# Kernel tuning notes

Measured on AMD Instinct MI355X. Metric: run time of the kernel, lower is better.

Reference implementation:

```python
import jax, jax.numpy as jnp
import numpy as np

NEG_SLOPE = 0.2


def gat_conv(x, src, dst, W, asrc, adst, b):
    """Single-head PyG-style GATConv with self-loops.
    x: [N, din], src/dst: [E] int, W: [din, d], asrc/adst: [d], b: [d]."""
    N = x.shape[0]
    h = x @ W  # [N, d]
    alpha_s = h @ asrc  # [N]
    alpha_d = h @ adst  # [N]
    # add self loops so every node has at least one incoming edge
    loop = jnp.arange(N, dtype=src.dtype)
    srcf = jnp.concatenate([src, loop])
    dstf = jnp.concatenate([dst, loop])
    e = jax.nn.leaky_relu(alpha_s[srcf] + alpha_d[dstf], NEG_SLOPE)  # [E+N]
    m = jax.ops.segment_max(e, dstf, num_segments=N)
    ex = jnp.exp(e - m[dstf])
    denom = jax.ops.segment_sum(ex, dstf, num_segments=N)
    alpha = ex / denom[dstf]
    out = jax.ops.segment_sum(h[srcf] * alpha[:, None], dstf, num_segments=N)
    return out + b


def sdgnn_forward(x, edges, Wg, a_src, a_dst, bg, W1, b1, W2, b2):
    L = Wg.shape[0]
    R = Wg.shape[1]
    for l in range(L):
        feats = [x]
        for r in range(R):
            feats.append(gat_conv(x, edges[r, 0], edges[r, 1],
                                  Wg[l, r], a_src[l, r], a_dst[l, r], bg[l, r]))
        combined = jnp.concatenate(feats, axis=1)  # [N, 5*d]
        x = jnp.tanh(combined @ W1[l] + b1[l]) @ W2[l] + b2[l]
    return x


def setup_inputs() -> dict:
    key = jax.random.key(0)
    ks = jax.random.split(key, 8)
    N, D, E, L, R = 100000, 64, 1000000, 2, 4
    scale = 0.15  # ~kaiming for d=64
    x = jax.random.normal(ks[0], (N, D), dtype=jnp.float32)
    edges = jax.random.randint(ks[1], (R, 2, E), 0, N, dtype=jnp.int64)
    Wg = jax.random.normal(ks[2], (L, R, D, D), dtype=jnp.float32) * scale
    a_src = jax.random.normal(ks[3], (L, R, D), dtype=jnp.float32) * scale
    a_dst = jax.random.normal(ks[4], (L, R, D), dtype=jnp.float32) * scale
    bg = jnp.zeros((L, R, D), dtype=jnp.float32)
    W1 = jax.random.normal(ks[5], (L, 5 * D, D), dtype=jnp.float32) * 0.08
    b1 = jnp.zeros((L, D), dtype=jnp.float32)
    W2 = jax.random.normal(ks[6], (L, D, D), dtype=jnp.float32) * scale
    b2 = jnp.zeros((L, D), dtype=jnp.float32)
    return {"x": x, "edges": edges, "Wg": Wg, "a_src": a_src, "a_dst": a_dst,
            "bg": bg, "W1": W1, "b1": b1, "W2": W2, "b2": b2}


def reference(x, edges, Wg, a_src, a_dst, bg, W1, b1, W2, b2):
    return sdgnn_forward(x, edges, Wg, a_src, a_dst, bg, W1, b1, W2, b2)
```

## Files before the change

### kernel.cpp

```cpp
#include <hip/hip_runtime.h>
#include <hip/hip_bf16.h>
#include <math.h>

#define DD 64
#define RREL 4
#define LLAY 2
#define NEG_SLOPE 0.2f
#define EPB 4096
#define BSH 10
#define BSZ 1024

typedef __attribute__((ext_vector_type(8))) short short8;
typedef __attribute__((ext_vector_type(4))) short short4v;
typedef __attribute__((ext_vector_type(4))) float float4v;

__device__ __forceinline__ float lrelu(float x) { return x > 0.f ? x : NEG_SLOPE * x; }

__device__ __forceinline__ unsigned short f2bf(float f) {
    unsigned int u = __float_as_uint(f);
    return (unsigned short)((u + 0x7FFFu + ((u >> 16) & 1u)) >> 16);
}
__device__ __forceinline__ float bf2f(unsigned short u) {
    return __uint_as_float((unsigned int)u << 16);
}

__global__ void k_wvec(const float* __restrict__ Wg, const float* __restrict__ asrc,
                       const float* __restrict__ adst, float* __restrict__ wsrc,
                       float* __restrict__ wdst) {
    int idx = blockIdx.x * blockDim.x + threadIdx.x;
    if (idx >= LLAY * RREL * DD) return;
    int k = idx & 63;
    int lr = idx >> 6;
    const float* W = Wg + (size_t)lr * DD * DD;
    const float* as = asrc + lr * DD;
    const float* ad = adst + lr * DD;
    float s1 = 0.f, s2 = 0.f;
#pragma unroll
    for (int j = 0; j < DD; j++) {
        float w = W[k * DD + j];
        s1 += w * as[j];
        s2 += w * ad[j];
    }
    wsrc[idx] = s1;
    wdst[idx] = s2;
}

__global__ void k_prep(const float* __restrict__ Wg, const float* __restrict__ W1,
                       const float* __restrict__ W2, unsigned short* __restrict__ WgT,
                       unsigned short* __restrict__ W1T, unsigned short* __restrict__ W2T) {
    int idx = blockIdx.x * blockDim.x + threadIdx.x;
    if (idx < 8 * 4096) {
        int lr = idx >> 12, rem = idx & 4095, n = rem >> 6, k = rem & 63;
        WgT[idx] = f2bf(Wg[(size_t)lr * 4096 + k * 64 + n]);
    } else if (idx < 32768 + 2 * 64 * 320) {
        int i = idx - 32768;
        int l = i / 20480, rem = i % 20480, n = rem / 320, kk = rem % 320;
        int src;
        if (kk < 64) src = kk;
        else {
            int r = (kk - 64) >> 6, f = (kk - 64) & 63;
            src = 64 + r * 64 + ((f & 3) * 16) + (f >> 2);
        }
        W1T[i] = f2bf(W1[(size_t)l * 20480 + src * 64 + n]);
    } else if (idx < 32768 + 40960 + 2 * 4096) {
        int i = idx - 73728;
        int l = i >> 12, rem = i & 4095, n = rem >> 6, k = rem & 63;
        W2T[i] = f2bf(W2[(size_t)l * 4096 + k * 64 + n]);
    }
}

__global__ void k_copy_x(const float* __restrict__ x, unsigned short* __restrict__ combined,
                         int N) {
    int i = blockIdx.x * blockDim.x + threadIdx.x;
    if (i >= N * 32) return;
    int row = i >> 5, c2 = i & 31;
    float2 v = *(const float2*)(x + (size_t)row * DD + c2 * 2);
    unsigned int p = (unsigned int)f2bf(v.x) | ((unsigned int)f2bf(v.y) << 16);
    *(unsigned int*)(combined + (size_t)row * 320 + c2 * 2) = p;
}

__global__ void k_zero(int* __restrict__ p, int n) {
    int i = blockIdx.x * blockDim.x + threadIdx.x;
    if (i < n) p[i] = 0;
}

__global__ __launch_bounds__(256) void k_bhist(const int* __restrict__ edges,
                                               int* __restrict__ btot, int E, int NB) {
    int r = blockIdx.y;
    int e0 = blockIdx.x * EPB;
    int t = threadIdx.x;
    __shared__ int lh[128];
    for (int i = t; i < 128; i += 256) lh[i] = 0;
    __syncthreads();
    const int* dstp = edges + (size_t)r * 2 * E + E;
#pragma unroll
    for (int i = 0; i < EPB / 256; i++) {
        int e = e0 + t + 256 * i;
        if (e < E) atomicAdd(&lh[dstp[e] >> BSH], 1);
    }
    __syncthreads();
    for (int i = t; i < NB; i += 256) {
        int c = lh[i];
        if (c) atomicAdd(&btot[r * NB + i], c);
    }
}

__global__ void k_bscan(const int* __restrict__ btot, int* __restrict__ bucketoff,
                        int* __restrict__ bpos, int* __restrict__ csr_ptr, int N, int E, int NB) {
    int r = threadIdx.x;
    if (r >= RREL) return;
    int run = 0;
    for (int b = 0; b < NB; b++) {
        bucketoff[r * (NB + 1) + b] = run;
        bpos[r * NB + b] = run;
        run += btot[r * NB + b];
    }
    bucketoff[r * (NB + 1) + NB] = run;
    csr_ptr[(size_t)r * (N + 1) + N] = E;
}

__global__ __launch_bounds__(256) void k_binscatter(const int* __restrict__ edges,
                                                    int* __restrict__ bpos,
                                                    unsigned int* __restrict__ packed, int E,
                                                    int NB) {
    int r = blockIdx.y;
    int e0 = blockIdx.x * EPB;
    int t = threadIdx.x;
    __shared__ int lh[128], lbase[128];
    for (int i = t; i < 128; i += 256) lh[i] = 0;
    __syncthreads();
    const int* srcp = edges + (size_t)r * 2 * E;
    const int* dstp = srcp + E;
    int md[EPB / 256], ms[EPB / 256];
#pragma unroll
    for (int i = 0; i < EPB / 256; i++) {
        int e = e0 + t + 256 * i;
        int d = -1, s = 0;
        if (e < E) {
            d = dstp[e];
            s = srcp[e];
            atomicAdd(&lh[d >> BSH], 1);
        }
        md[i] = d;
        ms[i] = s;
    }
    __syncthreads();
    for (int i = t; i < NB; i += 256) {
        int c = lh[i];
        lbase[i] = c ? atomicAdd(&bpos[r * NB + i], c) : 0;
        lh[i] = 0;
    }
    __syncthreads();
#pragma unroll
    for (int i = 0; i < EPB / 256; i++) {
        if (md[i] >= 0) {
            int b = md[i] >> BSH;
            int p = lbase[b] + atomicAdd(&lh[b], 1);
            packed[(size_t)r * E + p] =
                ((unsigned int)(md[i] & (BSZ - 1)) << 17) | (unsigned int)ms[i];
        }
    }
}

__global__ __launch_bounds__(256) void k_bucket_sort(const unsigned int* __restrict__ packed,
                                                     const int* __restrict__ bucketoff,
                                                     int* __restrict__ csr_ptr,
                                                     int* __restrict__ csr_src, int N, int E,
                                                     int NB) {
    int r = blockIdx.y, b = blockIdx.x;
    int t = threadIdx.x;
    __shared__ int pos[BSZ];
    __shared__ int tsum[256];
    int base = bucketoff[r * (NB + 1) + b];
    int cnt = bucketoff[r * (NB + 1) + b + 1] - base;
    const unsigned int* pk = packed + (size_t)r * E + base;
    for (int i = t; i < BSZ; i += 256) pos[i] = 0;
    __syncthreads();
    for (int i = t; i < cnt; i += 256) atomicAdd(&pos[pk[i] >> 17], 1);
    __syncthreads();
    int v[4];
    int s = 0;
#pragma unroll
    for (int i = 0; i < 4; i++) {
        v[i] = pos[t * 4 + i];
        s += v[i];
    }
    tsum[t] = s;
    __syncthreads();
    for (int off = 1; off < 256; off <<= 1) {
        int add = (t >= off) ? tsum[t - off] : 0;
        __syncthreads();
        tsum[t] += add;
        __syncthreads();
    }
    int run = tsum[t] - s;
    __syncthreads();
#pragma unroll
    for (int i = 0; i < 4; i++) {
        int node_l = t * 4 + i;
        pos[node_l] = run;
        int node = b * BSZ + node_l;
        if (node < N) csr_ptr[(size_t)r * (N + 1) + node] = base + run;
        run += v[i];
    }
    __syncthreads();
    for (int i = t; i < cnt; i += 256) {
        unsigned int p = pk[i];
        int d = p >> 17;
        int sidx = p & 0x1FFFF;
        int loc = atomicAdd(&pos[d], 1);
        csr_src[(size_t)r * E + base + loc] = sidx;
    }
}


__global__ __launch_bounds__(256, 3) void k_hgemm(const unsigned short* __restrict__ X,
                                                  const unsigned short* __restrict__ WgTl,
                                                  const float* __restrict__ wsrcl,
                                                  const float* __restrict__ wdstl,
                                                  unsigned short* __restrict__ h4,
                                                  float* __restrict__ as4,
                                                  float* __restrict__ ad4, int N) {
    __shared__ __align__(16) unsigned short Xb[256][72];
    __shared__ __align__(16) unsigned short Wb[64][72];
    __shared__ float wsS[4][64], wdS[4][64];
    int tid = threadIdx.x, wave = tid >> 6, lane = tid & 63;
    int l15 = lane & 15, q = lane >> 4;
    int row0 = blockIdx.x * 256;
#pragma unroll
    for (int i = 0; i < 8; i++) {
        int f = tid + 256 * i;
        int rr = f >> 3, seg = f & 7;
        int grow = row0 + rr;
        short8 v = (short8){0, 0, 0, 0, 0, 0, 0, 0};
        if (grow < N) v = *(const short8*)(X + (size_t)grow * 320 + seg * 8);
        *(short8*)&Xb[rr][seg * 8] = v;
    }
    wsS[tid >> 6][tid & 63] = wsrcl[tid];
    wdS[tid >> 6][tid & 63] = wdstl[tid];
    __syncthreads();
    short8 afr[4][2];
#pragma unroll
    for (int mt = 0; mt < 4; mt++)
#pragma unroll
        for (int ks = 0; ks < 2; ks++)
            afr[mt][ks] = *(const short8*)&Xb[wave * 64 + mt * 16 + l15][ks * 32 + q * 8];
    {
        int grow = row0 + tid;
        float s[4] = {0.f, 0.f, 0.f, 0.f}, d[4] = {0.f, 0.f, 0.f, 0.f};
#pragma unroll
        for (int seg = 0; seg < 8; seg++) {
            short8 v = *(const short8*)&Xb[tid][seg * 8];
#pragma unroll
            for (int j = 0; j < 8; j++) {
                float xv = bf2f((unsigned short)v[j]);
                int k = seg * 8 + j;
#pragma unroll
                for (int r = 0; r < 4; r++) {
                    s[r] += xv * wsS[r][k];
                    d[r] += xv * wdS[r][k];
                }
            }
        }
        if (grow < N) {
#pragma unroll
            for (int r = 0; r < 4; r++) {
                as4[(size_t)r * N + grow] = s[r];
                ad4[(size_t)r * N + grow] = d[r];
            }
        }
    }
    for (int r = 0; r < 4; r++) {
        __syncthreads();
#pragma unroll
        for (int i = 0; i < 2; i++) {
            int f = tid + 256 * i;
            int n = f >> 3, seg = f & 7;
            *(short8*)&Wb[n][seg * 8] = *(const short8*)(WgTl + r * 4096 + n * 64 + seg * 8);
        }
        __syncthreads();
        short8 bfr[4][2];
#pragma unroll
        for (int nt = 0; nt < 4; nt++)
#pragma unroll
            for (int ks = 0; ks < 2; ks++)
                bfr[nt][ks] = *(const short8*)&Wb[nt * 16 + l15][ks * 32 + q * 8];
        float4v acc[4][4];
#pragma unroll
        for (int mt = 0; mt < 4; mt++)
#pragma unroll
            for (int nt = 0; nt < 4; nt++) acc[mt][nt] = (float4v){0.f, 0.f, 0.f, 0.f};
#pragma unroll
        for (int mt = 0; mt < 4; mt++)
#pragma unroll
            for (int nt = 0; nt < 4; nt++) {
                acc[mt][nt] = __builtin_amdgcn_mfma_f32_16x16x32_bf16(afr[mt][0], bfr[nt][0],
                                                                     acc[mt][nt], 0, 0, 0);
                acc[mt][nt] = __builtin_amdgcn_mfma_f32_16x16x32_bf16(afr[mt][1], bfr[nt][1],
                                                                     acc[mt][nt], 0, 0, 0);
            }
        unsigned short* hr = h4 + (size_t)r * N * 64;
#pragma unroll
        for (int mt = 0; mt < 4; mt++) {
            int rowb = row0 + wave * 64 + mt * 16 + q * 4;
#pragma unroll
            for (int reg = 0; reg < 4; reg++) {
                int row = rowb + reg;
                if (row < N) {
                    short4v sv;
                    sv[0] = (short)f2bf(acc[mt][0][reg]);
                    sv[1] = (short)f2bf(acc[mt][1][reg]);
                    sv[2] = (short)f2bf(acc[mt][2][reg]);
                    sv[3] = (short)f2bf(acc[mt][3][reg]);
                    *(short4v*)&hr[(size_t)row * 64 + l15 * 4] = sv;
                }
            }
        }
    }
}

template <bool BFOUT>
__global__ __launch_bounds__(256, 3) void k_mlp(const unsigned short* __restrict__ X,
                                                const unsigned short* __restrict__ W1Tl,
                                                const float* __restrict__ b1,
                                                const unsigned short* __restrict__ W2Tl,
                                                const float* __restrict__ b2,
                                                unsigned short* __restrict__ Ybf,
                                                float* __restrict__ Yf, int ldy, int N) {
    __shared__ __align__(16) unsigned short Xb[256][72];
    __shared__ __align__(16) unsigned short Wb[64][72];
    int tid = threadIdx.x, wave = tid >> 6, lane = tid & 63;
    int l15 = lane & 15, q = lane >> 4;
    int row0 = blockIdx.x * 256;
    float4v acc[4][4];
#pragma unroll
    for (int mt = 0; mt < 4; mt++)
#pragma unroll
        for (int nt = 0; nt < 4; nt++) acc[mt][nt] = (float4v){0.f, 0.f, 0.f, 0.f};
    for (int kc = 0; kc < 320; kc += 64) {
        __syncthreads();
#pragma unroll
        for (int i = 0; i < 8; i++) {
            int f = tid + 256 * i;
            int rr = f >> 3, seg = f & 7;
            int grow = row0 + rr;
            short8 v = (short8){0, 0, 0, 0, 0, 0, 0, 0};
            if (grow < N) v = *(const short8*)(X + (size_t)grow * 320 + kc + seg * 8);
            *(short8*)&Xb[rr][seg * 8] = v;
        }
#pragma unroll
        for (int i = 0; i < 2; i++) {
            int f = tid + 256 * i;
            int n = f >> 3, seg = f & 7;
            *(short8*)&Wb[n][seg * 8] = *(const short8*)(W1Tl + n * 320 + kc + seg * 8);
        }
        __syncthreads();
        short8 bfr[4][2];
#pragma unroll
        for (int nt = 0; nt < 4; nt++)
#pragma unroll
            for (int ks = 0; ks < 2; ks++)
                bfr[nt][ks] = *(const short8*)&Wb[nt * 16 + l15][ks * 32 + q * 8];
#pragma unroll
        for (int mt = 0; mt < 4; mt++) {
            short8 a0 = *(const short8*)&Xb[wave * 64 + mt * 16 + l15][q * 8];
            short8 a1 = *(const short8*)&Xb[wave * 64 + mt * 16 + l15][32 + q * 8];
#pragma unroll
            for (int nt = 0; nt < 4; nt++) {
                acc[mt][nt] =
                    __builtin_amdgcn_mfma_f32_16x16x32_bf16(a0, bfr[nt][0], acc[mt][nt], 0, 0, 0);
                acc[mt][nt] =
                    __builtin_amdgcn_mfma_f32_16x16x32_bf16(a1, bfr[nt][1], acc[mt][nt], 0, 0, 0);
            }
        }
    }
    __syncthreads();
#pragma unroll
    for (int mt = 0; mt < 4; mt++) {
        int rlb = wave * 64 + mt * 16 + q * 4;
#pragma unroll
        for (int reg = 0; reg < 4; reg++) {
#pragma unroll
            for (int nt = 0; nt < 4; nt++) {
                int n = nt * 16 + l15;
                Xb[rlb + reg][n] = f2bf(tanhf(acc[mt][nt][reg] + b1[n]));
            }
        }
    }
#pragma unroll
    for (int i = 0; i < 2; i++) {
        int f = tid + 256 * i;
        int n = f >> 3, seg = f & 7;
        *(short8*)&Wb[n][seg * 8] = *(const short8*)(W2Tl + n * 64 + seg * 8);
    }
    __syncthreads();
    short8 bfr[4][2];
#pragma unroll
    for (int nt = 0; nt < 4; nt++)
#pragma unroll
        for (int ks = 0; ks < 2; ks++)
            bfr[nt][ks] = *(const short8*)&Wb[nt * 16 + l15][ks * 32 + q * 8];
    float4v acc2[4][4];
#pragma unroll
    for (int mt = 0; mt < 4; mt++)
#pragma unroll
        for (int nt = 0; nt < 4; nt++) acc2[mt][nt] = (float4v){0.f, 0.f, 0.f, 0.f};
#pragma unroll
    for (int mt = 0; mt < 4; mt++) {
        short8 a0 = *(const short8*)&Xb[wave * 64 + mt * 16 + l15][q * 8];
        short8 a1 = *(const short8*)&Xb[wave * 64 + mt * 16 + l15][32 + q * 8];
#pragma unroll
        for (int nt = 0; nt < 4; nt++) {
            acc2[mt][nt] =
                __builtin_amdgcn_mfma_f32_16x16x32_bf16(a0, bfr[nt][0], acc2[mt][nt], 0, 0, 0);
            acc2[mt][nt] =
                __builtin_amdgcn_mfma_f32_16x16x32_bf16(a1, bfr[nt][1], acc2[mt][nt], 0, 0, 0);
        }
    }
#pragma unroll
    for (int mt = 0; mt < 4; mt++) {
        int rowb = row0 + wave * 64 + mt * 16 + q * 4;
#pragma unroll
        for (int reg = 0; reg < 4; reg++) {
            int row = rowb + reg;
            if (row < N) {
#pragma unroll
                for (int nt = 0; nt < 4; nt++) {
                    int n = nt * 16 + l15;
                    float v = acc2[mt][nt][reg] + b2[n];
                    if (BFOUT)
                        Ybf[(size_t)row * ldy + n] = f2bf(v);
                    else
                        Yf[(size_t)row * ldy + n] = v;
                }
            }
        }
    }
}

__device__ void gat_node_fullwave(int node, const int* __restrict__ csr_ptr,
                                  const int* __restrict__ csr_src,
                                  const unsigned short* __restrict__ h,
                                  const float* __restrict__ as_,
                                  const float* __restrict__ ad_, float bgv,
                                  unsigned short* __restrict__ out, int ldo, int lane) {
    float adv = ad_[node];
    float e_self = lrelu(as_[node] + adv);
    int beg = csr_ptr[node], end = csr_ptr[node + 1];
    int cnt = end - beg;

    if (cnt <= 64) {
        int s = 0;
        float e_lane = -3.0e38f;
        if (lane < cnt) {
            s = csr_src[beg + lane];
            e_lane = lrelu(as_[s] + adv);
        }
        float m = fmaxf(e_lane, e_self);
#pragma unroll
        for (int off = 32; off; off >>= 1) m = fmaxf(m, __shfl_xor(m, off));
        float p = (lane < cnt) ? expf(e_lane - m) : 0.f;
        float ssum = p;
#pragma unroll
        for (int off = 32; off; off >>= 1) ssum += __shfl_xor(ssum, off);
        float p_self = expf(e_self - m);
        float inv = 1.f / (ssum + p_self);
        float alpha = p * inv;
        float acc = p_self * inv * bf2f(h[(size_t)node * DD + lane]);
        for (int j0 = 0; j0 < cnt; ++j0) {
            int ss = __shfl(s, j0);
            float aa = __shfl(alpha, j0);
            acc += aa * bf2f(h[(size_t)ss * DD + lane]);
        }
        out[(size_t)node * ldo + lane] = f2bf(acc + bgv);
        return;
    }

    float m = e_self;
    for (int j = beg + lane; j < end; j += 64) m = fmaxf(m, lrelu(as_[csr_src[j]] + adv));
#pragma unroll
    for (int off = 32; off; off >>= 1) m = fmaxf(m, __shfl_xor(m, off));
    float ssum = 0.f;
    for (int j = beg + lane; j < end; j += 64) ssum += expf(lrelu(as_[csr_src[j]] + adv) - m);
#pragma unroll
    for (int off = 32; off; off >>= 1) ssum += __shfl_xor(ssum, off);
    ssum += expf(e_self - m);
    float inv = 1.f / ssum;
    float acc = expf(e_self - m) * inv * bf2f(h[(size_t)node * DD + lane]);
    for (int j0 = beg; j0 < end; j0 += 64) {
        int j = j0 + lane;
        int s = 0;
        float alpha = 0.f;
        if (j < end) {
            s = csr_src[j];
            alpha = expf(lrelu(as_[s] + adv) - m) * inv;
        }
        int c = end - j0;
        if (c > 64) c = 64;
        for (int t = 0; t < c; ++t) {
            int ss = __shfl(s, t);
            float aa = __shfl(alpha, t);
            acc += aa * bf2f(h[(size_t)ss * DD + lane]);
        }
    }
    out[(size_t)node * ldo + lane] = f2bf(acc + bgv);
}

__global__ __launch_bounds__(256) void k_gat(const int* __restrict__ csr_ptr4,
                                             const int* __restrict__ csr_src4,
                                             const unsigned short* __restrict__ h4,
                                             const float* __restrict__ as4,
                                             const float* __restrict__ ad4,
                                             const float* __restrict__ bg4,
                                             unsigned short* __restrict__ outbase, int ldo,
                                             int N, int E) {
    __shared__ int lsa_s[4][2][32];
    __shared__ float lsa_p[4][2][32];
    int lb = blockIdx.x;
    int r = (lb & 7) >> 1;
    int idx = ((lb >> 3) << 1) + (lb & 1);
    int wave = threadIdx.x >> 6, lane = threadIdx.x & 63;
    int half = lane >> 5, lh = lane & 31;
    int nodeA = idx * 8 + wave * 2;
    if (nodeA >= N) return;
    int node = nodeA + half;
    bool act = node < N;

    const int* csr_ptr = csr_ptr4 + (size_t)r * (N + 1);
    const int* csr_src = csr_src4 + (size_t)r * E;
    const unsigned short* h = h4 + (size_t)r * N * 64;
    const float* as_ = as4 + (size_t)r * N;
    const float* ad_ = ad4 + (size_t)r * N;
    const float* bg = bg4 + (size_t)r * DD;
    unsigned short* out = outbase + (size_t)64 * r;

    int beg = 0, cnt = 0;
    if (act) {
        beg = csr_ptr[node];
        cnt = csr_ptr[node + 1] - beg;
    }
    int vmax = __builtin_amdgcn_readfirstlane(max(cnt, __shfl_xor(cnt, 32)));

    if (vmax <= 32) {
        bool in = lh < cnt;
        int s = 0;
        if (in) s = csr_src[beg + lh];
        lsa_s[wave][half][lh] = s;
        float adv = act ? ad_[node] : 0.f;
        float asl = in ? as_[s] : 0.f;
        float e_self = act ? lrelu(as_[node] + adv) : 0.f;
        float p = in ? __expf(lrelu(asl + adv)) : 0.f;
        lsa_p[wave][half][lh] = p;
        float p_self = __expf(e_self);

        const char* hb = (const char*)h;
        unsigned lane4 = (unsigned)(lh << 2);
        unsigned int hvs = 0;
        if (act) hvs = *(const unsigned int*)(hb + (((unsigned)node) << 7) + lane4);

        float ax0 = 0.f, ay0 = 0.f, ax1 = 0.f, ay1 = 0.f;
        const int* sp = &lsa_s[wave][half][0];
        const float* pp = &lsa_p[wave][half][0];
        for (int j0 = 0; j0 < vmax; j0 += 8) {
#pragma unroll
            for (int g = 0; g < 2; g++) {
                if (j0 + g * 4 < vmax) {
#pragma unroll
                    for (int u = 0; u < 4; u++) {
                        int sv = sp[j0 + g * 4 + u];
                        unsigned voff = ((unsigned)sv << 7) + lane4;
                        unsigned int hv = *(const unsigned int*)(hb + voff);
                        float pw = pp[j0 + g * 4 + u];
                        if (u & 1) {
                            ax1 += pw * __uint_as_float(hv << 16);
                            ay1 += pw * __uint_as_float(hv & 0xffff0000u);
                        } else {
                            ax0 += pw * __uint_as_float(hv << 16);
                            ay0 += pw * __uint_as_float(hv & 0xffff0000u);
                        }
                    }
                }
            }
        }
        float ssum = p;
#pragma unroll
        for (int off = 16; off; off >>= 1) ssum += __shfl_xor(ssum, off);
        float inv = __builtin_amdgcn_rcpf(ssum + p_self);

        if (act) {
            int f0 = 2 * lh;
            float bx = bg[((f0 & 3) << 4) | (f0 >> 2)];
            float by = bg[(((f0 + 1) & 3) << 4) | (f0 >> 2)];
            float ox = (ax0 + ax1 + p_self * __uint_as_float(hvs << 16)) * inv + bx;
            float oy = (ay0 + ay1 + p_self * __uint_as_float(hvs & 0xffff0000u)) * inv + by;
            unsigned int pck = (unsigned int)f2bf(ox) | ((unsigned int)f2bf(oy) << 16);
            *(unsigned int*)(out + (size_t)node * ldo + f0) = pck;
        }
        return;
    }

    float bgv = bg[((lane & 3) << 4) | (lane >> 2)];
    if (nodeA < N)
        gat_node_fullwave(nodeA, csr_ptr, csr_src, h, as_, ad_, bgv, out, ldo, lane);
    if (nodeA + 1 < N)
        gat_node_fullwave(nodeA + 1, csr_ptr, csr_src, h, as_, ad_, bgv, out, ldo, lane);
}

extern "C" void kernel_launch(void* const* d_in, const int* in_sizes, int n_in,
                              void* d_out, int out_size, void* d_ws, size_t ws_size,
                              hipStream_t stream) {
    const float* x = (const float*)d_in[0];
    const int* edges = (const int*)d_in[1];
    const float* Wg = (const float*)d_in[2];
    const float* a_src = (const float*)d_in[3];
    const float* a_dst = (const float*)d_in[4];
    const float* bg = (const float*)d_in[5];
    const float* W1 = (const float*)d_in[6];
    const float* b1 = (const float*)d_in[7];
    const float* W2 = (const float*)d_in[8];
    const float* b2 = (const float*)d_in[9];
    float* out = (float*)d_out;

    const int N = in_sizes[0] / DD;
    const int E = in_sizes[1] / (2 * RREL);
    const int NB = (N + BSZ - 1) >> BSH;

    size_t off = 0;
    auto alloc = [&](size_t bytes) {
        size_t o = off;
        off = (off + bytes + 255) & ~(size_t)255;
        return o;
    };
    char* ws = (char*)d_ws;
    unsigned short* combined = (unsigned short*)(ws + alloc((size_t)N * 320 * 2));
    unsigned short* h4 = (unsigned short*)(ws + alloc((size_t)4 * N * 64 * 2));
    float* wsrc = (float*)(ws + alloc(LLAY * RREL * DD * 4));
    float* wdst = (float*)(ws + alloc(LLAY * RREL * DD * 4));
    unsigned short* WgT = (unsigned short*)(ws + alloc(8 * 4096 * 2));
    unsigned short* W1T = (unsigned short*)(ws + alloc(2 * 64 * 320 * 2));
    unsigned short* W2T = (unsigned short*)(ws + alloc(2 * 4096 * 2));
    int* btot = (int*)(ws + alloc((size_t)RREL * NB * 4));
    int* bucketoff = (int*)(ws + alloc((size_t)RREL * (NB + 1) * 4));
    int* bpos = (int*)(ws + alloc((size_t)RREL * NB * 4));
    unsigned int* packed = (unsigned int*)(ws + alloc((size_t)RREL * E * 4));
    int* csr_ptr = (int*)(ws + alloc((size_t)RREL * (N + 1) * 4));
    int* csr_src = (int*)(ws + alloc((size_t)RREL * E * 4));
    (void)ws_size;
    float* as4 = (float*)packed;
    float* ad4 = as4 + (size_t)4 * N;

    const int ebblocks = (E + EPB - 1) / EPB;

    k_zero<<<dim3((RREL * NB + 255) / 256), dim3(256), 0, stream>>>(btot, RREL * NB);
    k_wvec<<<dim3(2), dim3(256), 0, stream>>>(Wg, a_src, a_dst, wsrc, wdst);
    k_prep<<<dim3(320), dim3(256), 0, stream>>>(Wg, W1, W2, WgT, W1T, W2T);
    k_copy_x<<<dim3((N * 32 + 255) / 256), dim3(256), 0, stream>>>(x, combined, N);
    k_bhist<<<dim3(ebblocks, RREL), dim3(256), 0, stream>>>(edges, btot, E, NB);
    k_bscan<<<dim3(1), dim3(64), 0, stream>>>(btot, bucketoff, bpos, csr_ptr, N, E, NB);
    k_binscatter<<<dim3(ebblocks, RREL), dim3(256), 0, stream>>>(edges, bpos, packed, E, NB);
    k_bucket_sort<<<dim3(NB, RREL), dim3(256), 0, stream>>>(packed, bucketoff, csr_ptr, csr_src,
                                                            N, E, NB);

    const int gemm_blocks = (N + 255) / 256;
    const int bpr = (N + 7) / 8;
    const int gat_grid = 8 * ((bpr + 1) / 2);

    for (int l = 0; l < LLAY; l++) {
        k_hgemm<<<dim3(gemm_blocks), dim3(256), 0, stream>>>(
            combined, WgT + (size_t)l * 4 * 4096, wsrc + l * 256, wdst + l * 256, h4, as4, ad4, N);
        k_gat<<<dim3(gat_grid), dim3(256), 0, stream>>>(
            csr_ptr, csr_src, h4, as4, ad4, bg + (size_t)l * RREL * DD,
            combined + 64, 320, N, E);
        if (l == LLAY - 1) {
            k_mlp<false><<<dim3(gemm_blocks), dim3(256), 0, stream>>>(
                combined, W1T + (size_t)l * 20480, b1 + l * DD, W2T + (size_t)l * 4096,
                b2 + l * DD, nullptr, out, DD, N);
        } else {
            k_mlp<true><<<dim3(gemm_blocks), dim3(256), 0, stream>>>(
                combined, W1T + (size_t)l * 20480, b1 + l * DD, W2T + (size_t)l * 4096,
                b2 + l * DD, combined, nullptr, 320, N);
        }
    }
}
```

Before: 504.3 us.

## Map 16 nodes per wave with 4 lanes per node in GAT aggregation

Restructures the GAT aggregation kernel so each wave handles 16 destination nodes, with 4 lanes per node each loading 32 bytes (two 16-byte vectors) of the bf16 feature row and keeping 16 accumulators. Previously each half-wave handled one node with 4-byte loads per lane. The aim is wider gather loads, fewer waves and better latency hiding per gathered edge. The cost is higher register pressure, more serial edge iterations per lane, and a wave-wide max degree that makes waves with skewed degrees do more work or fall back to the full-wave path for all 16 nodes. Output stores are now non-temporal 16-byte writes.

```diff
diff --git a/kernel.cpp b/kernel.cpp
--- a/kernel.cpp
+++ b/kernel.cpp
@@ -13,6 +13,7 @@
 typedef __attribute__((ext_vector_type(8))) short short8;
 typedef __attribute__((ext_vector_type(4))) short short4v;
 typedef __attribute__((ext_vector_type(4))) float float4v;
+typedef __attribute__((ext_vector_type(4))) unsigned int uint4v;
 
 __device__ __forceinline__ float lrelu(float x) { return x > 0.f ? x : NEG_SLOPE * x; }
 
@@ -22,6 +23,10 @@
 }
 __device__ __forceinline__ float bf2f(unsigned short u) {
     return __uint_as_float((unsigned int)u << 16);
+}
+__device__ __forceinline__ float bflo(unsigned int u) { return __uint_as_float(u << 16); }
+__device__ __forceinline__ float bfhi(unsigned int u) {
+    return __uint_as_float(u & 0xffff0000u);
 }
 
 __global__ void k_wvec(const float* __restrict__ Wg, const float* __restrict__ asrc,
@@ -514,16 +519,16 @@
                                              const float* __restrict__ bg4,
                                              unsigned short* __restrict__ outbase, int ldo,
                                              int N, int E) {
-    __shared__ int lsa_s[4][2][32];
-    __shared__ float lsa_p[4][2][32];
+    __shared__ int lsa_s[4][32][16];
+    __shared__ float lsa_p[4][32][16];
     int lb = blockIdx.x;
     int r = (lb & 7) >> 1;
     int idx = ((lb >> 3) << 1) + (lb & 1);
     int wave = threadIdx.x >> 6, lane = threadIdx.x & 63;
-    int half = lane >> 5, lh = lane & 31;
-    int nodeA = idx * 8 + wave * 2;
+    int quad = lane >> 2, lq = lane & 3;
+    int nodeA = idx * 64 + wave * 16;
     if (nodeA >= N) return;
-    int node = nodeA + half;
+    int node = nodeA + quad;
     bool act = node < N;
 
     const int* csr_ptr = csr_ptr4 + (size_t)r * (N + 1);
@@ -539,71 +544,130 @@
         beg = csr_ptr[node];
         cnt = csr_ptr[node + 1] - beg;
     }
-    int vmax = __builtin_amdgcn_readfirstlane(max(cnt, __shfl_xor(cnt, 32)));
+    int m2 = max(cnt, __shfl_xor(cnt, 4));
+    m2 = max(m2, __shfl_xor(m2, 8));
+    m2 = max(m2, __shfl_xor(m2, 16));
+    int vmax = __builtin_amdgcn_readfirstlane(max(m2, __shfl_xor(m2, 32)));
 
     if (vmax <= 32) {
-        bool in = lh < cnt;
-        int s = 0;
-        if (in) s = csr_src[beg + lh];
-        lsa_s[wave][half][lh] = s;
+        int sarr[8];
+        bool inarr[8];
+#pragma unroll
+        for (int t = 0; t < 8; t++) {
+            sarr[t] = 0;
+            inarr[t] = false;
+            if (vmax > 4 * t) {
+                int e = 4 * t + lq;
+                inarr[t] = e < cnt;
+                if (inarr[t]) sarr[t] = csr_src[beg + e];
+                lsa_s[wave][4 * t + lq][quad] = sarr[t];
+            }
+        }
         float adv = act ? ad_[node] : 0.f;
-        float asl = in ? as_[s] : 0.f;
         float e_self = act ? lrelu(as_[node] + adv) : 0.f;
-        float p = in ? __expf(lrelu(asl + adv)) : 0.f;
-        lsa_p[wave][half][lh] = p;
+        float psum = 0.f;
+#pragma unroll
+        for (int t = 0; t < 8; t++) {
+            if (vmax > 4 * t) {
+                float p = inarr[t] ? __expf(lrelu(as_[sarr[t]] + adv)) : 0.f;
+                lsa_p[wave][4 * t + lq][quad] = p;
+                psum += p;
+            }
+        }
         float p_self = __expf(e_self);
 
         const char* hb = (const char*)h;
-        unsigned lane4 = (unsigned)(lh << 2);
-        unsigned int hvs = 0;
-        if (act) hvs = *(const unsigned int*)(hb + (((unsigned)node) << 7) + lane4);
-
-        float ax0 = 0.f, ay0 = 0.f, ax1 = 0.f, ay1 = 0.f;
-        const int* sp = &lsa_s[wave][half][0];
-        const float* pp = &lsa_p[wave][half][0];
+        unsigned lane32 = (unsigned)(lq << 5);
+        uint4v hs1 = (uint4v){0u, 0u, 0u, 0u}, hs2 = (uint4v){0u, 0u, 0u, 0u};
+        if (act) {
+            hs1 = *(const uint4v*)(hb + (((unsigned)node) << 7) + lane32);
+            hs2 = *(const uint4v*)(hb + (((unsigned)node) << 7) + lane32 + 16);
+        }
+
+        float acc[16];
+#pragma unroll
+        for (int i = 0; i < 16; i++) acc[i] = 0.f;
+        const int(*sp)[16] = &lsa_s[wave][0];
+        const float(*pp)[16] = &lsa_p[wave][0];
         for (int j0 = 0; j0 < vmax; j0 += 8) {
 #pragma unroll
             for (int g = 0; g < 2; g++) {
                 if (j0 + g * 4 < vmax) {
 #pragma unroll
                     for (int u = 0; u < 4; u++) {
-                        int sv = sp[j0 + g * 4 + u];
-                        unsigned voff = ((unsigned)sv << 7) + lane4;
-                        unsigned int hv = *(const unsigned int*)(hb + voff);
-                        float pw = pp[j0 + g * 4 + u];
-                        if (u & 1) {
-                            ax1 += pw * __uint_as_float(hv << 16);
-                            ay1 += pw * __uint_as_float(hv & 0xffff0000u);
-                        } else {
-                            ax0 += pw * __uint_as_float(hv << 16);
-                            ay0 += pw * __uint_as_float(hv & 0xffff0000u);
-                        }
+                        int sv = sp[j0 + g * 4 + u][quad];
+                        unsigned base = ((unsigned)sv << 7) + lane32;
+                        uint4v h1 = *(const uint4v*)(hb + base);
+                        uint4v h2 = *(const uint4v*)(hb + base + 16);
+                        float pw = pp[j0 + g * 4 + u][quad];
+                        acc[0] += pw * bflo(h1.x);
+                        acc[1] += pw * bfhi(h1.x);
+                        acc[2] += pw * bflo(h1.y);
+                        acc[3] += pw * bfhi(h1.y);
+                        acc[4] += pw * bflo(h1.z);
+                        acc[5] += pw * bfhi(h1.z);
+                        acc[6] += pw * bflo(h1.w);
+                        acc[7] += pw * bfhi(h1.w);
+                        acc[8] += pw * bflo(h2.x);
+                        acc[9] += pw * bfhi(h2.x);
+                        acc[10] += pw * bflo(h2.y);
+                        acc[11] += pw * bfhi(h2.y);
+                        acc[12] += pw * bflo(h2.z);
+                        acc[13] += pw * bfhi(h2.z);
+                        acc[14] += pw * bflo(h2.w);
+                        acc[15] += pw * bfhi(h2.w);
                     }
                 }
             }
         }
-        float ssum = p;
-#pragma unroll
-        for (int off = 16; off; off >>= 1) ssum += __shfl_xor(ssum, off);
+        float ssum = psum;
+        ssum += __shfl_xor(ssum, 2);
+        ssum += __shfl_xor(ssum, 1);
         float inv = __builtin_amdgcn_rcpf(ssum + p_self);
 
         if (act) {
-            int f0 = 2 * lh;
-            float bx = bg[((f0 & 3) << 4) | (f0 >> 2)];
-            float by = bg[(((f0 + 1) & 3) << 4) | (f0 >> 2)];
-            float ox = (ax0 + ax1 + p_self * __uint_as_float(hvs << 16)) * inv + bx;
-            float oy = (ay0 + ay1 + p_self * __uint_as_float(hvs & 0xffff0000u)) * inv + by;
-            unsigned int pck = (unsigned int)f2bf(ox) | ((unsigned int)f2bf(oy) << 16);
-            *(unsigned int*)(out + (size_t)node * ldo + f0) = pck;
+            float4v bq0 = *(const float4v*)(bg + 4 * lq);
+            float4v bq1 = *(const float4v*)(bg + 16 + 4 * lq);
+            float4v bq2 = *(const float4v*)(bg + 32 + 4 * lq);
+            float4v bq3 = *(const float4v*)(bg + 48 + 4 * lq);
+            float hself[16];
+            hself[0] = bflo(hs1.x); hself[1] = bfhi(hs1.x);
+            hself[2] = bflo(hs1.y); hself[3] = bfhi(hs1.y);
+            hself[4] = bflo(hs1.z); hself[5] = bfhi(hs1.z);
+            hself[6] = bflo(hs1.w); hself[7] = bfhi(hs1.w);
+            hself[8] = bflo(hs2.x); hself[9] = bfhi(hs2.x);
+            hself[10] = bflo(hs2.y); hself[11] = bfhi(hs2.y);
+            hself[12] = bflo(hs2.z); hself[13] = bfhi(hs2.z);
+            hself[14] = bflo(hs2.w); hself[15] = bfhi(hs2.w);
+            unsigned int w[8];
+#pragma unroll
+            for (int i = 0; i < 16; i += 2) {
+                float bi, bj;
+                {
+                    int a = i >> 2;
+                    float4v* bqs[4] = {&bq0, &bq1, &bq2, &bq3};
+                    bi = (*bqs[i & 3])[a];
+                    bj = (*bqs[(i + 1) & 3])[a];
+                }
+                float oi = (acc[i] + p_self * hself[i]) * inv + bi;
+                float oj = (acc[i + 1] + p_self * hself[i + 1]) * inv + bj;
+                w[i >> 1] = (unsigned int)f2bf(oi) | ((unsigned int)f2bf(oj) << 16);
+            }
+            uint4v pck1 = (uint4v){w[0], w[1], w[2], w[3]};
+            uint4v pck2 = (uint4v){w[4], w[5], w[6], w[7]};
+            unsigned short* op = out + (size_t)node * ldo + 16 * lq;
+            __builtin_nontemporal_store(pck1, (uint4v*)op);
+            __builtin_nontemporal_store(pck2, (uint4v*)(op + 8));
         }
         return;
     }
 
     float bgv = bg[((lane & 3) << 4) | (lane >> 2)];
-    if (nodeA < N)
-        gat_node_fullwave(nodeA, csr_ptr, csr_src, h, as_, ad_, bgv, out, ldo, lane);
-    if (nodeA + 1 < N)
-        gat_node_fullwave(nodeA + 1, csr_ptr, csr_src, h, as_, ad_, bgv, out, ldo, lane);
+#pragma unroll
+    for (int k = 0; k < 16; k++) {
+        if (nodeA + k < N)
+            gat_node_fullwave(nodeA + k, csr_ptr, csr_src, h, as_, ad_, bgv, out, ldo, lane);
+    }
 }
 
 extern "C" void kernel_launch(void* const* d_in, const int* in_sizes, int n_in,
@@ -662,7 +726,7 @@
                                                             N, E, NB);
 
     const int gemm_blocks = (N + 255) / 256;
-    const int bpr = (N + 7) / 8;
+    const int bpr = (N + 63) / 64;
     const int gat_grid = 8 * ((bpr + 1) / 2);
 
     for (int l = 0; l < LLAY; l++) {
```

New measurement: 484.6 us. 1.04x faster.
